# Performance work log

Hardware: AMD Instinct MI355X
Metric: run time of the kernel (lower is better)

## Reference

```python
import jax, jax.numpy as jnp
import numpy as np
from jax import lax

B, CIN, H, W = 32, 256, 56, 56
COUT, M, K = 256, 2, 3
CMID = COUT * M  # 512
SPARSITY = 0.9


def _make_binary_weight(key):
    k1, k2 = jax.random.split(key)
    shape = (CMID, CIN, K, K)
    mask = jax.random.bernoulli(k1, SPARSITY, shape)
    sign = jax.random.bernoulli(k2, 0.5, shape).astype(jnp.float32) * 2.0 - 1.0
    return jnp.where(mask, sign, 0.0).astype(jnp.float32)


def setup_inputs() -> dict:
    key = jax.random.key(0)
    kx, kw, kfw, kfb = jax.random.split(key, 4)
    x = jax.random.normal(kx, (B, CIN, H, W), dtype=jnp.float32)
    binary_w = _make_binary_weight(kw)
    fan_in = CMID  # 1x1 conv fan-in
    bound = 1.0 / np.sqrt(fan_in)
    fc_w = jax.random.uniform(kfw, (COUT, CMID, 1, 1), minval=-bound, maxval=bound, dtype=jnp.float32)
    fc_b = jax.random.uniform(kfb, (COUT,), minval=-bound, maxval=bound, dtype=jnp.float32)
    return {"x": x, "binary_w": binary_w, "fc_w": fc_w, "fc_b": fc_b}


def reference(x, binary_w, fc_w, fc_b):
    pad = K // 2
    # fixed random ternary conv, stride 1, same padding
    y = lax.conv_general_dilated(
        x, binary_w, window_strides=(1, 1), padding=[(pad, pad), (pad, pad)],
        dimension_numbers=("NCHW", "OIHW", "NCHW"))
    y = jax.nn.relu(y)
    # learnable 1x1 conv with bias
    y = lax.conv_general_dilated(
        y, fc_w, window_strides=(1, 1), padding=[(0, 0), (0, 0)],
        dimension_numbers=("NCHW", "OIHW", "NCHW"))
    return y + fc_b[None, :, None, None]
```

## Files before the change

kernel.cpp:

```cpp
#include <hip/hip_runtime.h>
#include <hip/hip_bf16.h>
#include <stdint.h>


typedef __attribute__((ext_vector_type(8))) short short8;
typedef __attribute__((ext_vector_type(4))) float floatx4;

#define ROWE 8192
#define NT_PER_B 28

#define OFF_WP  0
#define OFF_A2  2359296
#define OFF_XP  2621440
#define OFF_Y   63439872

__device__ static inline void async16(const void* gptr, void* lptr) {
  __builtin_amdgcn_global_load_lds(
      (const __attribute__((address_space(1))) void*)gptr,
      (__attribute__((address_space(3))) void*)lptr,
      16, 0, 0);
}

__device__ static inline unsigned short f2bf(float x) {
  __hip_bfloat16 h = __float2bfloat16(x);
  return *reinterpret_cast<unsigned short*>(&h);
}

__global__ void k_xprep(const float* __restrict__ x, __hip_bfloat16* __restrict__ Xp) {
  const int t = blockIdx.x * 256 + threadIdx.x;
  const int wq  = t & 63;
  const int khi = (t >> 6) & 15;
  const int t2  = t >> 10;
  const int hp  = t2 % 58;
  const int bc  = t2 / 58;
  const int b   = bc >> 1;
  const int cin0 = ((bc & 1) << 7) + (khi << 3);
  const int h = hp - 1, w = wq - 1;
  unsigned short v[8];
  if ((unsigned)h < 56u && (unsigned)w < 56u) {
    const float* xp = x + ((size_t)(b * 256 + cin0) * 56 + h) * 56 + w;
#pragma unroll
    for (int j = 0; j < 8; ++j) v[j] = f2bf(xp[(size_t)j * 3136]);
  } else {
#pragma unroll
    for (int j = 0; j < 8; ++j) v[j] = 0;
  }
  uint4 pk;
  pk.x = (unsigned)v[0] | ((unsigned)v[1] << 16);
  pk.y = (unsigned)v[2] | ((unsigned)v[3] << 16);
  pk.z = (unsigned)v[4] | ((unsigned)v[5] << 16);
  pk.w = (unsigned)v[6] | ((unsigned)v[7] << 16);
  *(uint4*)(Xp + (size_t)t * 8) = pk;
}

__global__ void k_wprep(const float* __restrict__ bw, __hip_bfloat16* __restrict__ Wp) {
  const int idx = blockIdx.x * 256 + threadIdx.x;
  const int klo = idx & 7;
  const int cml = (idx >> 3) & 63;
  const int khi = (idx >> 9) & 15;
  const int cmh = (idx >> 13) & 1;
  const int rest = idx >> 14;
  const int cmblk = rest & 3;
  const int tcg = rest >> 2;
  const int cg  = tcg & 1;
  const int tap = tcg >> 1;
  const int kh = tap / 3, kw = tap - kh * 3;
  const int cm  = (cmblk << 7) + (cmh << 6) + cml;
  const int cin = (cg << 7) + (khi << 3) + klo;
  Wp[idx] = __float2bfloat16(bw[((cm * 256 + cin) * 3 + kh) * 3 + kw]);
}

__global__ void k_a2prep(const float* __restrict__ fw, __hip_bfloat16* __restrict__ A2) {
  const int idx = blockIdx.x * 256 + threadIdx.x;
  const int klo = idx & 7;
  const int cl  = (idx >> 3) & 63;
  const int khi = (idx >> 9) & 15;
  const int ch  = (idx >> 13) & 1;
  const int rest = idx >> 14;
  const int mtile = rest & 1;
  const int cg = rest >> 1;
  const int cout = (mtile << 7) + (ch << 6) + cl;
  const int cm   = (cg << 7) + (khi << 3) + klo;
  A2[idx] = __float2bfloat16(fw[cout * 512 + cm]);
}

__global__ __launch_bounds__(256, 2) void k_conv1(
    const __hip_bfloat16* __restrict__ Xp, const __hip_bfloat16* __restrict__ Wp,
    __hip_bfloat16* __restrict__ Y) {
  __shared__ short8 lds_raw[4096];
  char* lds = (char*)lds_raw;
  const int tid  = threadIdx.x;
  const int lane = tid & 63;
  const int wv   = tid >> 6;
  const int wm   = wv >> 1, wn = wv & 1;
  const int l15  = lane & 15;
  const int quad = lane >> 4;
  const int id   = blockIdx.x;
  const int xcd  = id & 7;
  const int seq  = id >> 3;
  const int cmblk = seq & 3;
  const int ntile = xcd * 112 + (seq >> 2);
  const int b  = ntile / NT_PER_B;
  const int h0 = (ntile % NT_PER_B) * 2;

  floatx4 acc[4][4];
#pragma unroll
  for (int i = 0; i < 4; i++)
#pragma unroll
    for (int j = 0; j < 4; j++) acc[i][j] = (floatx4){0.f, 0.f, 0.f, 0.f};

  for (int t = 0; t < 18; ++t) {
    const int tap = t >> 1;
    const int cg  = t & 1;
    const int kh = tap / 3, kw = tap - kh * 3;
    const size_t a_base = (size_t)((tap * 2 + cg) * 4 + cmblk) * 16384;
    const size_t b_base = (size_t)((b * 2 + cg) * 58 + (h0 + kh)) * ROWE + kw * 8;
    __syncthreads();
    const char* gA = (const char*)(Wp + a_base) + wv * 8192 + lane * 16;
    const char* gB = (const char*)(Xp + b_base) + wv * 8192 + lane * 16;
    char* lA = lds + wv * 8192;
    char* lB = lds + 32768 + wv * 8192;
#pragma unroll
    for (int c = 0; c < 8; ++c) {
      async16(gA + c * 1024, lA + c * 1024);
      async16(gB + c * 1024, lB + c * 1024);
    }
    __syncthreads();
#pragma unroll
    for (int kk = 0; kk < 4; ++kk) {
      short8 af[4], bf[4];
#pragma unroll
      for (int mi = 0; mi < 4; ++mi) {
        const int m = wm * 64 + mi * 16 + l15;
        af[mi] = *(const short8*)(lds + ((m >> 6) * 16 + kk * 4 + quad) * 1024 + (m & 63) * 16);
      }
#pragma unroll
      for (int ni = 0; ni < 4; ++ni) {
        const int n = wn * 64 + ni * 16 + l15;
        bf[ni] = *(const short8*)(lds + 32768 + ((n >> 6) * 16 + kk * 4 + quad) * 1024 + (n & 63) * 16);
      }
#pragma unroll
      for (int mi = 0; mi < 4; ++mi)
#pragma unroll
        for (int ni = 0; ni < 4; ++ni)
          acc[mi][ni] = __builtin_amdgcn_mfma_f32_16x16x32_bf16(af[mi], bf[ni], acc[mi][ni], 0, 0, 0);
    }
  }

  const size_t ybase = ((size_t)ntile * 4 + cmblk) * 16384;
#pragma unroll
  for (int mi = 0; mi < 4; ++mi) {
    const int cml  = wm * 64 + mi * 16 + quad * 4;
    const int khi  = cml >> 3;
    const int klo0 = cml & 7;
#pragma unroll
    for (int ni = 0; ni < 4; ++ni) {
      const int n = wn * 64 + ni * 16 + l15;
      const int r = n >> 6, w = n & 63;
      floatx4 f = acc[mi][ni];
      unsigned lo = (unsigned)f2bf(fmaxf(f[0], 0.f)) | ((unsigned)f2bf(fmaxf(f[1], 0.f)) << 16);
      unsigned hi = (unsigned)f2bf(fmaxf(f[2], 0.f)) | ((unsigned)f2bf(fmaxf(f[3], 0.f)) << 16);
      uint2 pk = make_uint2(lo, hi);
      *(uint2*)((char*)Y + (ybase + (size_t)r * 8192 + khi * 512 + w * 8 + klo0) * 2) = pk;
    }
  }
}

__global__ __launch_bounds__(256, 2) void k_conv2(
    const __hip_bfloat16* __restrict__ Y, const __hip_bfloat16* __restrict__ A2,
    const float* __restrict__ fcb, float* __restrict__ out) {
  __shared__ short8 lds_raw[4096];
  char* lds = (char*)lds_raw;
  const int tid  = threadIdx.x;
  const int lane = tid & 63;
  const int wv   = tid >> 6;
  const int wm   = wv >> 1, wn = wv & 1;
  const int l15  = lane & 15;
  const int quad = lane >> 4;
  const int id   = blockIdx.x;
  const int xcd  = id & 7;
  const int seq  = id >> 3;
  const int mtile = seq & 1;
  const int rp    = xcd * 112 + (seq >> 1);

  floatx4 acc[4][4];
#pragma unroll
  for (int i = 0; i < 4; i++)
#pragma unroll
    for (int j = 0; j < 4; j++) acc[i][j] = (floatx4){0.f, 0.f, 0.f, 0.f};

  for (int cg = 0; cg < 4; ++cg) {
    const size_t a_base = (size_t)(cg * 2 + mtile) * 16384;
    const size_t b_base = (size_t)(rp * 4 + cg) * 16384;
    __syncthreads();
    const char* gA = (const char*)(A2 + a_base) + wv * 8192 + lane * 16;
    const char* gB = (const char*)(Y + b_base) + wv * 8192 + lane * 16;
    char* lA = lds + wv * 8192;
    char* lB = lds + 32768 + wv * 8192;
#pragma unroll
    for (int c = 0; c < 8; ++c) {
      async16(gA + c * 1024, lA + c * 1024);
      async16(gB + c * 1024, lB + c * 1024);
    }
    __syncthreads();
#pragma unroll
    for (int kk = 0; kk < 4; ++kk) {
      short8 af[4], bf[4];
#pragma unroll
      for (int mi = 0; mi < 4; ++mi) {
        const int m = wm * 64 + mi * 16 + l15;
        af[mi] = *(const short8*)(lds + ((m >> 6) * 16 + kk * 4 + quad) * 1024 + (m & 63) * 16);
      }
#pragma unroll
      for (int ni = 0; ni < 4; ++ni) {
        const int n = wn * 64 + ni * 16 + l15;
        bf[ni] = *(const short8*)(lds + 32768 + ((n >> 6) * 16 + kk * 4 + quad) * 1024 + (n & 63) * 16);
      }
#pragma unroll
      for (int mi = 0; mi < 4; ++mi)
#pragma unroll
        for (int ni = 0; ni < 4; ++ni)
          acc[mi][ni] = __builtin_amdgcn_mfma_f32_16x16x32_bf16(af[mi], bf[ni], acc[mi][ni], 0, 0, 0);
    }
  }

  const int b   = rp / NT_PER_B;
  const int nb0 = (rp % NT_PER_B) * 128;
#pragma unroll
  for (int mi = 0; mi < 4; ++mi) {
    const int co = mtile * 128 + wm * 64 + mi * 16 + quad * 4;
#pragma unroll
    for (int ni = 0; ni < 4; ++ni) {
      const int n = wn * 64 + ni * 16 + l15;
      const int w = n & 63;
      if (w < 56) {
        const int nb = nb0 + n;
        const int h  = nb >> 6;
        floatx4 f = acc[mi][ni];
        const size_t base = (size_t)(b * 256 + co) * 3136 + h * 56 + w;
#pragma unroll
        for (int r = 0; r < 4; ++r)
          out[base + (size_t)r * 3136] = f[r] + fcb[co + r];
      }
    }
  }
}

extern "C" void kernel_launch(void* const* d_in, const int* in_sizes, int n_in,
                              void* d_out, int out_size, void* d_ws, size_t ws_size,
                              hipStream_t stream) {
  const float* x  = (const float*)d_in[0];
  const float* bw = (const float*)d_in[1];
  const float* fw = (const float*)d_in[2];
  const float* fb = (const float*)d_in[3];
  float* out = (float*)d_out;
  char* ws = (char*)d_ws;

  __hip_bfloat16* Wp = (__hip_bfloat16*)(ws + OFF_WP);
  __hip_bfloat16* A2 = (__hip_bfloat16*)(ws + OFF_A2);
  __hip_bfloat16* Xp = (__hip_bfloat16*)(ws + OFF_XP);
  __hip_bfloat16* Y  = (__hip_bfloat16*)(ws + OFF_Y);

  k_wprep<<<dim3(4608), dim3(256), 0, stream>>>(bw, Wp);
  k_a2prep<<<dim3(512), dim3(256), 0, stream>>>(fw, A2);
  k_xprep<<<dim3(14848), dim3(256), 0, stream>>>(x, Xp);
  k_conv1<<<dim3(3584), dim3(256), 0, stream>>>(Xp, Wp, Y);
  k_conv2<<<dim3(1792), dim3(256), 0, stream>>>(Y, A2, fb, out);
}
```

Measured before the change: 481.1 us.

## Enlarge conv1 tile to 256x256 with double-buffered LDS and interleaved MFMA scheduling

Rewrites the first conv GEMM kernel so each 512-thread block computes a 256-channel by 4-row tile. Shared memory is double-buffered so the next K-step's global-to-LDS copies are issued while MFMAs run on the current buffer. Explicit sched barriers, setprio and partial vmcnt waits interleave the loads with the MFMA groups. This aims to raise data reuse per block and hide memory latency, at the cost of twice the LDS, more accumulator registers (128 floats per lane) and fewer blocks, which may lower occupancy.

```diff
diff --git a/kernel.cpp b/kernel.cpp
--- a/kernel.cpp
+++ b/kernel.cpp
@@ -84,84 +84,149 @@
   A2[idx] = __float2bfloat16(fw[cout * 512 + cm]);
 }
 
-__global__ __launch_bounds__(256, 2) void k_conv1(
+
+#define SB0 __builtin_amdgcn_sched_barrier(0)
+#define BARRIER do { SB0; __builtin_amdgcn_s_barrier(); SB0; } while (0)
+#define MM(A, B, C) __builtin_amdgcn_mfma_f32_16x16x32_bf16((A), (B), (C), 0, 0, 0)
+#define LD8(P) (*(const short8*)(P))
+
+#define MFMA16(MIH, NIH) do { \
+  __builtin_amdgcn_s_setprio(1); \
+  acc[(MIH)*4+0][(NIH)*2+0] = MM(a0, b0, acc[(MIH)*4+0][(NIH)*2+0]); \
+  acc[(MIH)*4+1][(NIH)*2+0] = MM(a1, b0, acc[(MIH)*4+1][(NIH)*2+0]); \
+  acc[(MIH)*4+2][(NIH)*2+0] = MM(a2, b0, acc[(MIH)*4+2][(NIH)*2+0]); \
+  acc[(MIH)*4+3][(NIH)*2+0] = MM(a3, b0, acc[(MIH)*4+3][(NIH)*2+0]); \
+  acc[(MIH)*4+0][(NIH)*2+1] = MM(a0, b1, acc[(MIH)*4+0][(NIH)*2+1]); \
+  acc[(MIH)*4+1][(NIH)*2+1] = MM(a1, b1, acc[(MIH)*4+1][(NIH)*2+1]); \
+  acc[(MIH)*4+2][(NIH)*2+1] = MM(a2, b1, acc[(MIH)*4+2][(NIH)*2+1]); \
+  acc[(MIH)*4+3][(NIH)*2+1] = MM(a3, b1, acc[(MIH)*4+3][(NIH)*2+1]); \
+  acc[(MIH)*4+0][(NIH)*2+0] = MM(p0, b2, acc[(MIH)*4+0][(NIH)*2+0]); \
+  acc[(MIH)*4+1][(NIH)*2+0] = MM(p1, b2, acc[(MIH)*4+1][(NIH)*2+0]); \
+  acc[(MIH)*4+2][(NIH)*2+0] = MM(p2, b2, acc[(MIH)*4+2][(NIH)*2+0]); \
+  acc[(MIH)*4+3][(NIH)*2+0] = MM(p3, b2, acc[(MIH)*4+3][(NIH)*2+0]); \
+  acc[(MIH)*4+0][(NIH)*2+1] = MM(p0, b3, acc[(MIH)*4+0][(NIH)*2+1]); \
+  acc[(MIH)*4+1][(NIH)*2+1] = MM(p1, b3, acc[(MIH)*4+1][(NIH)*2+1]); \
+  acc[(MIH)*4+2][(NIH)*2+1] = MM(p2, b3, acc[(MIH)*4+2][(NIH)*2+1]); \
+  acc[(MIH)*4+3][(NIH)*2+1] = MM(p3, b3, acc[(MIH)*4+3][(NIH)*2+1]); \
+  __builtin_amdgcn_s_setprio(0); \
+} while (0)
+
+__global__ __launch_bounds__(512, 2) void k_conv1(
     const __hip_bfloat16* __restrict__ Xp, const __hip_bfloat16* __restrict__ Wp,
     __hip_bfloat16* __restrict__ Y) {
-  __shared__ short8 lds_raw[4096];
+  __shared__ short8 lds_raw[8192];
   char* lds = (char*)lds_raw;
   const int tid  = threadIdx.x;
   const int lane = tid & 63;
   const int wv   = tid >> 6;
-  const int wm   = wv >> 1, wn = wv & 1;
+  const int wm   = wv >> 2;
+  const int wn   = wv & 3;
   const int l15  = lane & 15;
   const int quad = lane >> 4;
   const int id   = blockIdx.x;
   const int xcd  = id & 7;
   const int seq  = id >> 3;
-  const int cmblk = seq & 3;
-  const int ntile = xcd * 112 + (seq >> 2);
-  const int b  = ntile / NT_PER_B;
-  const int h0 = (ntile % NT_PER_B) * 2;
-
-  floatx4 acc[4][4];
-#pragma unroll
-  for (int i = 0; i < 4; i++)
+  const int mt   = seq & 1;
+  const int nt   = xcd * 56 + (seq >> 1);
+  const int b    = nt / 14;
+  const int h0   = (nt % 14) * 4;
+
+  const char* WpB = (const char*)Wp;
+  const char* XpB = (const char*)Xp;
+
+  const int thrA = ((wv & 3) << 11) + lane * 16;
+  const int aRd = wm * 16384 + quad * 1024 + l15 * 16;
+  const int bRd = wn * 8192 + quad * 1024 + l15 * 16;
+
+  floatx4 acc[8][4];
+#pragma unroll
+  for (int i = 0; i < 8; i++)
 #pragma unroll
     for (int j = 0; j < 4; j++) acc[i][j] = (floatx4){0.f, 0.f, 0.f, 0.f};
 
+  {
+    const char* gA = WpB + (size_t)(2 * mt + wm) * 32768 + thrA;
+    const char* gB = XpB + ((size_t)(b * 2) * 58 + h0 + wm) * 16384 + thrA;
+    char* sA = lds + wm * 16384 + thrA;
+    char* sB = lds + 32768 + wm * 8192 + thrA;
+    async16(gA, sA);                     async16(gA + 1024, sA + 1024);
+    async16(gB, sB);                     async16(gB + 1024, sB + 1024);
+    async16(gB + 32768, sB + 16384);     async16(gB + 32768 + 1024, sB + 16384 + 1024);
+    async16(gA + 16384, sA + 8192);      async16(gA + 16384 + 1024, sA + 8192 + 1024);
+    asm volatile("s_waitcnt vmcnt(2)" ::: "memory");
+    BARRIER;
+  }
+
+  auto STEP = [&](int BUF, const char* gA, const char* gB, bool pred) {
+    char* ldsC = lds + BUF * 65536;
+    char* ldsS = lds + (BUF ^ 1) * 65536;
+    const char* Ab = ldsC + aRd;
+    const char* Bb = ldsC + 32768 + bRd;
+    char* sA = ldsS + wm * 16384 + thrA;
+    char* sB = ldsS + 32768 + wm * 8192 + thrA;
+    short8 a0, a1, a2, a3, p0, p1, p2, p3, b0, b1, b2, b3;
+    a0 = LD8(Ab + 0);     a1 = LD8(Ab + 256);  a2 = LD8(Ab + 512);  a3 = LD8(Ab + 768);
+    p0 = LD8(Ab + 4096);  p1 = LD8(Ab + 4352); p2 = LD8(Ab + 4608); p3 = LD8(Ab + 4864);
+    b0 = LD8(Bb + 0);     b1 = LD8(Bb + 256);  b2 = LD8(Bb + 4096); b3 = LD8(Bb + 4352);
+    if (pred) { async16(gA, sA); async16(gA + 1024, sA + 1024); }
+    BARRIER;
+    MFMA16(0, 0);
+    BARRIER;
+    b0 = LD8(Bb + 512);   b1 = LD8(Bb + 768);  b2 = LD8(Bb + 4608); b3 = LD8(Bb + 4864);
+    if (pred) { async16(gB, sB); async16(gB + 1024, sB + 1024); }
+    BARRIER;
+    MFMA16(0, 1);
+    if (pred) asm volatile("s_waitcnt vmcnt(4)" ::: "memory");
+    else      asm volatile("s_waitcnt vmcnt(0)" ::: "memory");
+    BARRIER;
+    a0 = LD8(Ab + 8192);  a1 = LD8(Ab + 8448);  a2 = LD8(Ab + 8704);  a3 = LD8(Ab + 8960);
+    p0 = LD8(Ab + 12288); p1 = LD8(Ab + 12544); p2 = LD8(Ab + 12800); p3 = LD8(Ab + 13056);
+    b0 = LD8(Bb + 0);     b1 = LD8(Bb + 256);   b2 = LD8(Bb + 4096);  b3 = LD8(Bb + 4352);
+    if (pred) { async16(gB + 32768, sB + 16384); async16(gB + 32768 + 1024, sB + 16384 + 1024); }
+    BARRIER;
+    MFMA16(1, 0);
+    BARRIER;
+    b0 = LD8(Bb + 512);   b1 = LD8(Bb + 768);   b2 = LD8(Bb + 4608);  b3 = LD8(Bb + 4864);
+    if (pred) { async16(gA + 16384, sA + 8192); async16(gA + 16384 + 1024, sA + 8192 + 1024); }
+    BARRIER;
+    MFMA16(1, 1);
+    asm volatile("s_waitcnt vmcnt(2)" ::: "memory");
+    BARRIER;
+  };
+
   for (int t = 0; t < 18; ++t) {
+    const int cg  = t & 1;
     const int tap = t >> 1;
-    const int cg  = t & 1;
     const int kh = tap / 3, kw = tap - kh * 3;
-    const size_t a_base = (size_t)((tap * 2 + cg) * 4 + cmblk) * 16384;
-    const size_t b_base = (size_t)((b * 2 + cg) * 58 + (h0 + kh)) * ROWE + kw * 8;
-    __syncthreads();
-    const char* gA = (const char*)(Wp + a_base) + wv * 8192 + lane * 16;
-    const char* gB = (const char*)(Xp + b_base) + wv * 8192 + lane * 16;
-    char* lA = lds + wv * 8192;
-    char* lB = lds + 32768 + wv * 8192;
-#pragma unroll
-    for (int c = 0; c < 8; ++c) {
-      async16(gA + c * 1024, lA + c * 1024);
-      async16(gB + c * 1024, lB + c * 1024);
-    }
-    __syncthreads();
-#pragma unroll
-    for (int kk = 0; kk < 4; ++kk) {
-      short8 af[4], bf[4];
-#pragma unroll
-      for (int mi = 0; mi < 4; ++mi) {
-        const int m = wm * 64 + mi * 16 + l15;
-        af[mi] = *(const short8*)(lds + ((m >> 6) * 16 + kk * 4 + quad) * 1024 + (m & 63) * 16);
-      }
-#pragma unroll
-      for (int ni = 0; ni < 4; ++ni) {
-        const int n = wn * 64 + ni * 16 + l15;
-        bf[ni] = *(const short8*)(lds + 32768 + ((n >> 6) * 16 + kk * 4 + quad) * 1024 + (n & 63) * 16);
-      }
-#pragma unroll
-      for (int mi = 0; mi < 4; ++mi)
-#pragma unroll
-        for (int ni = 0; ni < 4; ++ni)
-          acc[mi][ni] = __builtin_amdgcn_mfma_f32_16x16x32_bf16(af[mi], bf[ni], acc[mi][ni], 0, 0, 0);
-    }
-  }
-
-  const size_t ybase = ((size_t)ntile * 4 + cmblk) * 16384;
-#pragma unroll
-  for (int mi = 0; mi < 4; ++mi) {
-    const int cml  = wm * 64 + mi * 16 + quad * 4;
+    const int tn   = t + 1;
+    const int cgn  = tn & 1;
+    const int tapn = tn >> 1;
+    const int khn = tapn / 3, kwn = tapn - khn * 3;
+    const char* gA1 = WpB + (size_t)(t * 4 + 2 * mt + wm) * 32768 + 8192 + thrA;
+    const char* gB1 = XpB + ((size_t)(b * 2 + cg) * 58 + h0 + kh + wm) * 16384 + kw * 16 + 8192 + thrA;
+    const char* gA0 = WpB + (size_t)(tn * 4 + 2 * mt + wm) * 32768 + thrA;
+    const char* gB0 = XpB + ((size_t)(b * 2 + cgn) * 58 + h0 + khn + wm) * 16384 + kwn * 16 + thrA;
+    STEP(0, gA1, gB1, true);
+    STEP(1, gA0, gB0, t < 17);
+  }
+
+  const int cmblk = mt * 2 + wm;
+  const int ntile = nt * 2 + (wn >> 1);
+  const int r2    = wn & 1;
+  const size_t ybase = (((size_t)ntile * 4 + cmblk) * 2 + r2) * 8192;
+#pragma unroll
+  for (int mi = 0; mi < 8; ++mi) {
+    const int cml  = mi * 16 + quad * 4;
     const int khi  = cml >> 3;
     const int klo0 = cml & 7;
 #pragma unroll
     for (int ni = 0; ni < 4; ++ni) {
-      const int n = wn * 64 + ni * 16 + l15;
-      const int r = n >> 6, w = n & 63;
+      const int w = ni * 16 + l15;
       floatx4 f = acc[mi][ni];
       unsigned lo = (unsigned)f2bf(fmaxf(f[0], 0.f)) | ((unsigned)f2bf(fmaxf(f[1], 0.f)) << 16);
       unsigned hi = (unsigned)f2bf(fmaxf(f[2], 0.f)) | ((unsigned)f2bf(fmaxf(f[3], 0.f)) << 16);
       uint2 pk = make_uint2(lo, hi);
-      *(uint2*)((char*)Y + (ybase + (size_t)r * 8192 + khi * 512 + w * 8 + klo0) * 2) = pk;
+      *(uint2*)((char*)Y + (ybase + (size_t)khi * 512 + w * 8 + klo0) * 2) = pk;
     }
   }
 }
@@ -264,6 +329,6 @@
   k_wprep<<<dim3(4608), dim3(256), 0, stream>>>(bw, Wp);
   k_a2prep<<<dim3(512), dim3(256), 0, stream>>>(fw, A2);
   k_xprep<<<dim3(14848), dim3(256), 0, stream>>>(x, Xp);
-  k_conv1<<<dim3(3584), dim3(256), 0, stream>>>(Xp, Wp, Y);
+  k_conv1<<<dim3(896), dim3(512), 0, stream>>>(Xp, Wp, Y);
   k_conv2<<<dim3(1792), dim3(256), 0, stream>>>(Y, A2, fb, out);
 }
```

Result: no change. 490.6 us (+2.0%).

## Double-buffer conv1 LDS loads and enlarge per-block M tile to 256

Applied to the files above, without the earlier changes.

Rewrites the conv1 implicit-GEMM main loop so each block computes 256 output channels by 128 pixels, halving the grid. Global-to-LDS async loads for the next K slice are issued into a second LDS buffer while MFMAs run on the current one, with a single barrier per iteration. Each wave now holds 8x4 accumulators and adds setprio and sched_barrier hints around the MFMA block. The larger tile raises register pressure and cuts block count, which may lower occupancy and affect load balance; the changed Wp/Xp indexing also assumes layouts produced by the prep kernels.

```diff
diff --git a/kernel.cpp b/kernel.cpp
--- a/kernel.cpp
+++ b/kernel.cpp
@@ -84,84 +84,118 @@
   A2[idx] = __float2bfloat16(fw[cout * 512 + cm]);
 }
 
+
+#define SB0 __builtin_amdgcn_sched_barrier(0)
+#define MM(A, B, C) __builtin_amdgcn_mfma_f32_16x16x32_bf16((A), (B), (C), 0, 0, 0)
+#define LD8(P) (*(const short8*)(P))
+
 __global__ __launch_bounds__(256, 2) void k_conv1(
     const __hip_bfloat16* __restrict__ Xp, const __hip_bfloat16* __restrict__ Wp,
     __hip_bfloat16* __restrict__ Y) {
-  __shared__ short8 lds_raw[4096];
+  __shared__ short8 lds_raw[3072];
   char* lds = (char*)lds_raw;
   const int tid  = threadIdx.x;
   const int lane = tid & 63;
   const int wv   = tid >> 6;
-  const int wm   = wv >> 1, wn = wv & 1;
+  const int wm   = wv >> 1;
+  const int wn   = wv & 1;
   const int l15  = lane & 15;
   const int quad = lane >> 4;
   const int id   = blockIdx.x;
   const int xcd  = id & 7;
   const int seq  = id >> 3;
-  const int cmblk = seq & 3;
-  const int ntile = xcd * 112 + (seq >> 2);
-  const int b  = ntile / NT_PER_B;
-  const int h0 = (ntile % NT_PER_B) * 2;
-
-  floatx4 acc[4][4];
-#pragma unroll
-  for (int i = 0; i < 4; i++)
+  const int mt   = seq & 1;
+  const int ntile = xcd * 112 + (seq >> 1);
+  const int b    = ntile / NT_PER_B;
+  const int h0   = (ntile % NT_PER_B) * 2;
+
+  const char* WpB = (const char*)Wp;
+  const char* XpB = (const char*)Xp;
+  const int thr16 = tid * 16;
+
+  const int aRd = wm * 8192 + quad * 1024 + l15 * 16;
+  const int bRd = 16384 + wn * 4096 + quad * 1024 + l15 * 16;
+
+  floatx4 acc[8][4];
+#pragma unroll
+  for (int i = 0; i < 8; i++)
 #pragma unroll
     for (int j = 0; j < 4; j++) acc[i][j] = (floatx4){0.f, 0.f, 0.f, 0.f};
 
-  for (int t = 0; t < 18; ++t) {
+  auto STAGE = [&](char* sbase, int t, int sp) {
+    const int cg  = t & 1;
     const int tap = t >> 1;
-    const int cg  = t & 1;
     const int kh = tap / 3, kw = tap - kh * 3;
-    const size_t a_base = (size_t)((tap * 2 + cg) * 4 + cmblk) * 16384;
-    const size_t b_base = (size_t)((b * 2 + cg) * 58 + (h0 + kh)) * ROWE + kw * 8;
-    __syncthreads();
-    const char* gA = (const char*)(Wp + a_base) + wv * 8192 + lane * 16;
-    const char* gB = (const char*)(Xp + b_base) + wv * 8192 + lane * 16;
-    char* lA = lds + wv * 8192;
-    char* lB = lds + 32768 + wv * 8192;
-#pragma unroll
-    for (int c = 0; c < 8; ++c) {
-      async16(gA + c * 1024, lA + c * 1024);
-      async16(gB + c * 1024, lB + c * 1024);
-    }
-    __syncthreads();
-#pragma unroll
-    for (int kk = 0; kk < 4; ++kk) {
-      short8 af[4], bf[4];
-#pragma unroll
-      for (int mi = 0; mi < 4; ++mi) {
-        const int m = wm * 64 + mi * 16 + l15;
-        af[mi] = *(const short8*)(lds + ((m >> 6) * 16 + kk * 4 + quad) * 1024 + (m & 63) * 16);
-      }
-#pragma unroll
-      for (int ni = 0; ni < 4; ++ni) {
-        const int n = wn * 64 + ni * 16 + l15;
-        bf[ni] = *(const short8*)(lds + 32768 + ((n >> 6) * 16 + kk * 4 + quad) * 1024 + (n & 63) * 16);
-      }
-#pragma unroll
-      for (int mi = 0; mi < 4; ++mi)
-#pragma unroll
-        for (int ni = 0; ni < 4; ++ni)
-          acc[mi][ni] = __builtin_amdgcn_mfma_f32_16x16x32_bf16(af[mi], bf[ni], acc[mi][ni], 0, 0, 0);
-    }
-  }
-
+#pragma unroll
+    for (int cb = 0; cb < 2; ++cb)
+#pragma unroll
+      for (int cmh = 0; cmh < 2; ++cmh)
+        async16(WpB + ((size_t)((t * 4 + mt * 2 + cb) * 2 + cmh)) * 16384
+                    + sp * 4096 + thr16,
+                sbase + (cb * 2 + cmh) * 4096 + thr16);
+#pragma unroll
+    for (int r = 0; r < 2; ++r)
+      async16(XpB + ((size_t)((b * 2 + cg) * 58 + h0 + kh + r)) * 16384
+                  + sp * 4096 + kw * 16 + thr16,
+              sbase + 16384 + r * 4096 + thr16);
+  };
+
+  STAGE(lds, 0, 0);
+  SB0;
+  asm volatile("s_waitcnt vmcnt(0)" ::: "memory");
+  __builtin_amdgcn_s_barrier();
+  SB0;
+
+  for (int j = 0; j < 72; ++j) {
+    char* ldsC = lds + (j & 1) * 24576;
+    char* ldsS = lds + ((j & 1) ^ 1) * 24576;
+    if (j < 71) STAGE(ldsS, (j + 1) >> 2, (j + 1) & 3);
+    SB0;
+    const char* Ab = ldsC + aRd;
+    const char* Bb = ldsC + bRd;
+    short8 a0, a1, a2, a3, a4, a5, a6, a7, b0, b1, b2, b3;
+    a0 = LD8(Ab + 0);    a1 = LD8(Ab + 256);  a2 = LD8(Ab + 512);  a3 = LD8(Ab + 768);
+    a4 = LD8(Ab + 4096); a5 = LD8(Ab + 4352); a6 = LD8(Ab + 4608); a7 = LD8(Ab + 4864);
+    b0 = LD8(Bb + 0);    b1 = LD8(Bb + 256);  b2 = LD8(Bb + 512);  b3 = LD8(Bb + 768);
+    __builtin_amdgcn_s_setprio(1);
+    acc[0][0] = MM(a0, b0, acc[0][0]);  acc[0][1] = MM(a0, b1, acc[0][1]);
+    acc[0][2] = MM(a0, b2, acc[0][2]);  acc[0][3] = MM(a0, b3, acc[0][3]);
+    acc[1][0] = MM(a1, b0, acc[1][0]);  acc[1][1] = MM(a1, b1, acc[1][1]);
+    acc[1][2] = MM(a1, b2, acc[1][2]);  acc[1][3] = MM(a1, b3, acc[1][3]);
+    acc[2][0] = MM(a2, b0, acc[2][0]);  acc[2][1] = MM(a2, b1, acc[2][1]);
+    acc[2][2] = MM(a2, b2, acc[2][2]);  acc[2][3] = MM(a2, b3, acc[2][3]);
+    acc[3][0] = MM(a3, b0, acc[3][0]);  acc[3][1] = MM(a3, b1, acc[3][1]);
+    acc[3][2] = MM(a3, b2, acc[3][2]);  acc[3][3] = MM(a3, b3, acc[3][3]);
+    acc[4][0] = MM(a4, b0, acc[4][0]);  acc[4][1] = MM(a4, b1, acc[4][1]);
+    acc[4][2] = MM(a4, b2, acc[4][2]);  acc[4][3] = MM(a4, b3, acc[4][3]);
+    acc[5][0] = MM(a5, b0, acc[5][0]);  acc[5][1] = MM(a5, b1, acc[5][1]);
+    acc[5][2] = MM(a5, b2, acc[5][2]);  acc[5][3] = MM(a5, b3, acc[5][3]);
+    acc[6][0] = MM(a6, b0, acc[6][0]);  acc[6][1] = MM(a6, b1, acc[6][1]);
+    acc[6][2] = MM(a6, b2, acc[6][2]);  acc[6][3] = MM(a6, b3, acc[6][3]);
+    acc[7][0] = MM(a7, b0, acc[7][0]);  acc[7][1] = MM(a7, b1, acc[7][1]);
+    acc[7][2] = MM(a7, b2, acc[7][2]);  acc[7][3] = MM(a7, b3, acc[7][3]);
+    __builtin_amdgcn_s_setprio(0);
+    SB0;
+    asm volatile("s_waitcnt vmcnt(0)" ::: "memory");
+    __builtin_amdgcn_s_barrier();
+    SB0;
+  }
+
+  const int cmblk = mt * 2 + wm;
   const size_t ybase = ((size_t)ntile * 4 + cmblk) * 16384;
 #pragma unroll
-  for (int mi = 0; mi < 4; ++mi) {
-    const int cml  = wm * 64 + mi * 16 + quad * 4;
+  for (int mi = 0; mi < 8; ++mi) {
+    const int cml  = mi * 16 + quad * 4;
     const int khi  = cml >> 3;
     const int klo0 = cml & 7;
 #pragma unroll
     for (int ni = 0; ni < 4; ++ni) {
-      const int n = wn * 64 + ni * 16 + l15;
-      const int r = n >> 6, w = n & 63;
+      const int w = ni * 16 + l15;
       floatx4 f = acc[mi][ni];
       unsigned lo = (unsigned)f2bf(fmaxf(f[0], 0.f)) | ((unsigned)f2bf(fmaxf(f[1], 0.f)) << 16);
       unsigned hi = (unsigned)f2bf(fmaxf(f[2], 0.f)) | ((unsigned)f2bf(fmaxf(f[3], 0.f)) << 16);
       uint2 pk = make_uint2(lo, hi);
-      *(uint2*)((char*)Y + (ybase + (size_t)r * 8192 + khi * 512 + w * 8 + klo0) * 2) = pk;
+      *(uint2*)((char*)Y + (ybase + (size_t)wn * 8192 + khi * 512 + w * 8 + klo0) * 2) = pk;
     }
   }
 }
@@ -264,6 +298,6 @@
   k_wprep<<<dim3(4608), dim3(256), 0, stream>>>(bw, Wp);
   k_a2prep<<<dim3(512), dim3(256), 0, stream>>>(fw, A2);
   k_xprep<<<dim3(14848), dim3(256), 0, stream>>>(x, Xp);
-  k_conv1<<<dim3(3584), dim3(256), 0, stream>>>(Xp, Wp, Y);
+  k_conv1<<<dim3(1792), dim3(256), 0, stream>>>(Xp, Wp, Y);
   k_conv2<<<dim3(1792), dim3(256), 0, stream>>>(Y, A2, fb, out);
 }
```

Measured after the change: 464.2 us. 1.04x faster.
